# Kernel optimization log

Measured on AMD Instinct MI355X. Metric: run time of the kernel, lower is better.

## Reference

```python
import jax, jax.numpy as jnp
import numpy as np

N = 50000      # nodes
E = 800000     # edges (before self loops)
HID = 128      # hidden_dim
FEAT = 128     # feat_dim
NEG_SLOPE = 0.2
BN_EPS = 1e-5


def setup_inputs() -> dict:
    key = jax.random.key(0)
    ks = jax.random.split(key, 16)
    s = lambda d: 1.0 / np.sqrt(d).astype(np.float32)
    return {
        "x": jax.random.normal(ks[0], (N, HID), jnp.float32),
        "edge_index": jax.random.randint(ks[1], (2, E), 0, N, jnp.int32),
        # GATConv 1 (hidden -> hidden)
        "W1": jax.random.normal(ks[2], (HID, HID), jnp.float32) * s(HID),
        "att_src1": jax.random.normal(ks[3], (HID,), jnp.float32) * s(HID),
        "att_dst1": jax.random.normal(ks[4], (HID,), jnp.float32) * s(HID),
        "b1": jnp.zeros((HID,), jnp.float32),
        # BatchNorm1d(hidden) -- eval mode buffers/params
        "bn_gamma": jnp.ones((HID,), jnp.float32),
        "bn_beta": jnp.zeros((HID,), jnp.float32),
        "bn_mean": jax.random.normal(ks[5], (HID,), jnp.float32) * 0.1,
        "bn_var": jax.random.uniform(ks[6], (HID,), jnp.float32, 0.5, 1.5),
        # GATConv 2 (hidden -> feat)
        "W2": jax.random.normal(ks[7], (HID, FEAT), jnp.float32) * s(HID),
        "att_src2": jax.random.normal(ks[8], (FEAT,), jnp.float32) * s(FEAT),
        "att_dst2": jax.random.normal(ks[9], (FEAT,), jnp.float32) * s(FEAT),
        "b2": jnp.zeros((FEAT,), jnp.float32),
    }


def _gat_conv(x, W, att_src, att_dst, bias, src, dst, n_nodes):
    """PyG GATConv, heads=1: gather -> edge attn -> segment softmax -> scatter."""
    h = x @ W                                   # [N, d_out]
    a_s = h @ att_src                           # [N]
    a_d = h @ att_dst                           # [N]
    e = jax.nn.leaky_relu(a_s[src] + a_d[dst], NEG_SLOPE)  # [E']
    # numerically-stable softmax over incoming edges of each dst node
    e_max = jax.ops.segment_max(e, dst, num_segments=n_nodes)
    ex = jnp.exp(e - e_max[dst])
    denom = jax.ops.segment_sum(ex, dst, num_segments=n_nodes)
    alpha = ex / (denom[dst] + 1e-16)           # [E']
    out = jax.ops.segment_sum(alpha[:, None] * h[src], dst, num_segments=n_nodes)
    return out + bias


def reference(x, edge_index, W1, att_src1, att_dst1, b1,
              bn_gamma, bn_beta, bn_mean, bn_var,
              W2, att_src2, att_dst2, b2):
    n = x.shape[0]
    loops = jnp.arange(n, dtype=edge_index.dtype)
    src = jnp.concatenate([edge_index[0], loops])
    dst = jnp.concatenate([edge_index[1], loops])

    h = jax.nn.relu(_gat_conv(x, W1, att_src1, att_dst1, b1, src, dst, n))
    # BatchNorm1d in eval mode (running stats); dropout is identity in eval
    h = (h - bn_mean) * jax.lax.rsqrt(bn_var + BN_EPS) * bn_gamma + bn_beta
    out = jax.nn.relu(_gat_conv(h, W2, att_src2, att_dst2, b2, src, dst, n))
    return out
```

## Files before the change

### kernel.cpp

```cpp
#include <hip/hip_runtime.h>

typedef unsigned short u16;
typedef unsigned int   u32;
typedef __attribute__((ext_vector_type(8))) short bh8;
typedef __attribute__((ext_vector_type(4))) float fx4;

#define SCAN_FLAG 0x40000000

__device__ __forceinline__ float b2f(u16 h){ return __uint_as_float(((u32)h) << 16); }
__device__ __forceinline__ u16   f2b(float f){
  u32 u = __float_as_uint(f);
  u32 r = u + 0x7FFFu + ((u >> 16) & 1u);
  return (u16)(r >> 16);
}
__device__ __forceinline__ float lo16(u32 w){ return b2f((u16)(w & 0xFFFFu)); }
__device__ __forceinline__ float hi16(u32 w){ return b2f((u16)(w >> 16)); }

__global__ void r26_zero(int* __restrict__ cnt, int n1, int* __restrict__ pub){
  int g = (int)blockIdx.x*256 + threadIdx.x;
  if (g < n1) cnt[g] = 0;
  else if (g < n1 + 256) pub[g - n1] = 0;
}

__global__ void r26_hist_prep(const int* __restrict__ ei, int E, int Ep, int* cnt,
                              u16* __restrict__ rank,
                              const float* __restrict__ W1, const float* __restrict__ as1,
                              const float* __restrict__ ad1,
                              const float* __restrict__ W2, const float* __restrict__ as2,
                              const float* __restrict__ ad2,
                              u16* __restrict__ w1H, u16* __restrict__ w1L,
                              u16* __restrict__ w2H, u16* __restrict__ w2L,
                              float* __restrict__ ws1, float* __restrict__ wd1,
                              float* __restrict__ ws2, float* __restrict__ wd2){
  int b = blockIdx.x;
  int t = threadIdx.x;
  if (b < 16){
    const float* W = (b < 8) ? W1 : W2;
    u16* HT = (b < 8) ? w1H : w2H;
    u16* LT = (b < 8) ? w1L : w2L;
    int n0 = (b & 7) * 16;
    #pragma unroll
    for (int it = 0; it < 8; ++it){
      int idx = it*256 + t;
      int nn = n0 + (idx >> 7);
      int k = idx & 127;
      float w = W[(size_t)k*128 + nn];
      u16 h = f2b(w);
      HT[(size_t)nn*128 + k] = h;
      LT[(size_t)nn*128 + k] = f2b(w - b2f(h));
    }
    return;
  }
  if (b == 16){
    int which = t >> 6;
    const float* W   = (which < 2) ? W1 : W2;
    const float* att = (which == 0) ? as1 : (which == 1) ? ad1 : (which == 2) ? as2 : ad2;
    float* outv      = (which == 0) ? ws1 : (which == 1) ? wd1 : (which == 2) ? ws2 : wd2;
    int k0 = (t & 63) * 2;
    #pragma unroll
    for (int kk = 0; kk < 2; ++kk){
      int k = k0 + kk;
      float s = 0.f;
      for (int c = 0; c < 128; ++c) s = fmaf(W[(size_t)k*128 + c], att[c], s);
      outv[k] = s;
    }
    return;
  }
  int g0 = (b - 17)*2048 + t;
  #pragma unroll
  for (int i = 0; i < 8; ++i){
    int g = g0 + i*256;
    if (g < Ep){
      int dst = (g < E) ? ei[E + g] : (g - E);
      int r = atomicAdd(&cnt[dst], 1);
      rank[g] = (u16)r;
    }
  }
}

__global__ __launch_bounds__(256)
void r26_scan(const int* __restrict__ cnt, int n, int* __restrict__ offs,
              int* __restrict__ pub){
  __shared__ int tmp[256];
  __shared__ int red[256];
  int t = threadIdx.x; int b = blockIdx.x; int g = b*256 + t;
  int v = (g < n) ? cnt[g] : 0;
  tmp[t] = v; __syncthreads();
  for (int off = 1; off < 256; off <<= 1){
    int u = (t >= off) ? tmp[t - off] : 0;
    __syncthreads();
    tmp[t] += u;
    __syncthreads();
  }
  int incl = tmp[t];
  if (t == 255) atomicExch(&pub[b], tmp[255] | SCAN_FLAG);
  int val = 0;
  if (t < b){
    int p;
    do { p = atomicAdd(&pub[t], 0); } while (!(p & SCAN_FLAG));
    val = p & ~SCAN_FLAG;
  }
  red[t] = val; __syncthreads();
  for (int off = 128; off >= 1; off >>= 1){
    if (t < off) red[t] += red[t + off];
    __syncthreads();
  }
  int add = red[0];
  if (g < n) offs[g] = add + incl - v;
}

__device__ __forceinline__ void gemm16_wave(
    const float* __restrict__ X, const u16* __restrict__ wH, const u16* __restrict__ wL,
    const float* __restrict__ wsv, const float* __restrict__ wdv,
    u16* __restrict__ HB, float* __restrict__ AS, float* __restrict__ AD,
    int nrows, int w, int lane)
{
  int r0 = w * 16;
  if (r0 >= nrows) return;
  int rloc = lane & 15;
  int q    = lane >> 4;
  int myrow = r0 + rloc;
  bool act = (myrow < nrows);
  int rsafe = act ? myrow : (nrows - 1);

  fx4 acc[8] = {};
  float ds = 0.f, dd = 0.f;

  const u16* wHrow = wH + (size_t)rloc * 128;
  const u16* wLrow = wL + (size_t)rloc * 128;

  #pragma unroll
  for (int kk = 0; kk < 4; ++kk){
    int kbase = kk*32 + q*8;
    const float* xp = X + (size_t)rsafe*128 + kbase;
    float4 xa = *(const float4*)xp;
    float4 xb = *(const float4*)(xp + 4);
    float xv[8] = {xa.x, xa.y, xa.z, xa.w, xb.x, xb.y, xb.z, xb.w};
    if (!act){
      #pragma unroll
      for (int i = 0; i < 8; ++i) xv[i] = 0.f;
    }
    const float* sp = wsv + kbase;
    const float* dp = wdv + kbase;
    bh8 xh, xl;
    #pragma unroll
    for (int i = 0; i < 8; ++i){
      ds = fmaf(xv[i], sp[i], ds);
      dd = fmaf(xv[i], dp[i], dd);
      u16 h = f2b(xv[i]);
      xh[i] = (short)h;
      xl[i] = (short)f2b(xv[i] - b2f(h));
    }
    #pragma unroll
    for (int cf = 0; cf < 8; ++cf){
      bh8 wh = *(const bh8*)(wHrow + (size_t)cf*2048 + kbase);
      bh8 wl = *(const bh8*)(wLrow + (size_t)cf*2048 + kbase);
      acc[cf] = __builtin_amdgcn_mfma_f32_16x16x32_bf16(wh, xh, acc[cf], 0, 0, 0);
      acc[cf] = __builtin_amdgcn_mfma_f32_16x16x32_bf16(wl, xh, acc[cf], 0, 0, 0);
      acc[cf] = __builtin_amdgcn_mfma_f32_16x16x32_bf16(wh, xl, acc[cf], 0, 0, 0);
    }
  }
  ds += __shfl_xor(ds, 16); ds += __shfl_xor(ds, 32);
  dd += __shfl_xor(dd, 16); dd += __shfl_xor(dd, 32);
  if (act && q == 0){ AS[myrow] = ds; AD[myrow] = dd; }
  if (act){
    u16* hrow = HB + (size_t)myrow*128 + q*4;
    #pragma unroll
    for (int cf = 0; cf < 8; ++cf){
      uint2 pb;
      pb.x = (u32)f2b(acc[cf][0]) | ((u32)f2b(acc[cf][1]) << 16);
      pb.y = (u32)f2b(acc[cf][2]) | ((u32)f2b(acc[cf][3]) << 16);
      *(uint2*)(hrow + cf*16) = pb;
    }
  }
}

__global__ __launch_bounds__(256)
void r26_gemm_fill(const float* __restrict__ X,
                   const u16* __restrict__ wH, const u16* __restrict__ wL,
                   const float* __restrict__ wsv, const float* __restrict__ wdv,
                   u16* __restrict__ HB, float* __restrict__ AS, float* __restrict__ AD,
                   int nrows, int gemmBlocks,
                   const int* __restrict__ ei, int E, int Ep,
                   const int* __restrict__ offs, const u16* __restrict__ rank,
                   u16* __restrict__ csr){
  int t = threadIdx.x;
  if ((int)blockIdx.x >= gemmBlocks){
    int g0 = ((int)blockIdx.x - gemmBlocks)*1024 + t;
    #pragma unroll
    for (int i = 0; i < 4; ++i){
      int g = g0 + i*256;
      if (g < Ep){
        int src, dst;
        if (g < E){ src = ei[g]; dst = ei[E + g]; } else { src = g - E; dst = g - E; }
        csr[offs[dst] + (int)rank[g]] = (u16)src;
      }
    }
    return;
  }
  int w = (int)blockIdx.x*4 + (t >> 6);
  gemm16_wave(X, wH, wL, wsv, wdv, HB, AS, AD, nrows, w, t & 63);
}

__global__ __launch_bounds__(1024)
void r26_fused(const u16* __restrict__ HB, const float* __restrict__ AS,
               const float* __restrict__ AD,
               const int* __restrict__ offs, const u16* __restrict__ csr,
               const float* __restrict__ bias,
               const float* __restrict__ gamma_, const float* __restrict__ beta_,
               const float* __restrict__ mean_, const float* __restrict__ var_,
               const u16* __restrict__ w2H, const u16* __restrict__ w2L,
               const float* __restrict__ ws2, const float* __restrict__ wd2,
               u16* __restrict__ HB2, float* __restrict__ AS2, float* __restrict__ AD2,
               int n){
  __shared__ float xs[16*132];
  int tid  = threadIdx.x;
  int w    = tid >> 6;
  int lane = tid & 63;
  int wid  = (int)blockIdx.x*16 + w;
  bool validNode = (wid < n);
  int h  = lane >> 5;
  int c4 = (lane & 31) * 4;
  float a0 = 0.f, a1 = 0.f, a2 = 0.f, a3 = 0.f;

  if (validNode){
    int beg = offs[wid], end = offs[wid+1];
    int deg = end - beg;
    float ad = AD[wid];
    if (deg <= 64){
      int   my_s = 0;
      float my_e = -3.0e38f;
      bool act = (lane < deg);
      if (act){
        my_s = (int)csr[beg + lane];
        float e = AS[my_s] + ad;
        my_e = (e > 0.f) ? e : 0.2f*e;
      }
      float m = my_e;
      #pragma unroll
      for (int off = 32; off >= 1; off >>= 1) m = fmaxf(m, __shfl_xor(m, off));
      float pz = act ? __expf(my_e - m) : 0.f;
      float den = pz;
      #pragma unroll
      for (int off = 32; off >= 1; off >>= 1) den += __shfl_xor(den, off);
      float my_al = pz / (den + 1e-16f);

      int npair = (deg + 1) >> 1;
      int k = 0;
      for (; k + 4 <= npair; k += 4){
        int j0 = 2*k + h, j1 = j0 + 2, j2 = j0 + 4, j3 = j0 + 6;
        int   s0 = __shfl(my_s, j0),  s1 = __shfl(my_s, j1);
        int   s2 = __shfl(my_s, j2),  s3 = __shfl(my_s, j3);
        float l0 = __shfl(my_al, j0), l1 = __shfl(my_al, j1);
        float l2 = __shfl(my_al, j2), l3 = __shfl(my_al, j3);
        uint2 q0 = *(const uint2*)&HB[(size_t)s0*128 + c4];
        uint2 q1 = *(const uint2*)&HB[(size_t)s1*128 + c4];
        uint2 q2 = *(const uint2*)&HB[(size_t)s2*128 + c4];
        uint2 q3 = *(const uint2*)&HB[(size_t)s3*128 + c4];
        a0 = fmaf(l0, lo16(q0.x), a0); a1 = fmaf(l0, hi16(q0.x), a1);
        a2 = fmaf(l0, lo16(q0.y), a2); a3 = fmaf(l0, hi16(q0.y), a3);
        a0 = fmaf(l1, lo16(q1.x), a0); a1 = fmaf(l1, hi16(q1.x), a1);
        a2 = fmaf(l1, lo16(q1.y), a2); a3 = fmaf(l1, hi16(q1.y), a3);
        a0 = fmaf(l2, lo16(q2.x), a0); a1 = fmaf(l2, hi16(q2.x), a1);
        a2 = fmaf(l2, lo16(q2.y), a2); a3 = fmaf(l2, hi16(q2.y), a3);
        a0 = fmaf(l3, lo16(q3.x), a0); a1 = fmaf(l3, hi16(q3.x), a1);
        a2 = fmaf(l3, lo16(q3.y), a2); a3 = fmaf(l3, hi16(q3.y), a3);
      }
      for (; k < npair; ++k){
        int j = 2*k + h;
        int   s = __shfl(my_s, j);
        float l = __shfl(my_al, j);
        uint2 q = *(const uint2*)&HB[(size_t)s*128 + c4];
        a0 = fmaf(l, lo16(q.x), a0); a1 = fmaf(l, hi16(q.x), a1);
        a2 = fmaf(l, lo16(q.y), a2); a3 = fmaf(l, hi16(q.y), a3);
      }
    } else {
      float m = -3.0e38f;
      for (int k = beg + lane; k < end; k += 64){
        int s = (int)csr[k];
        float e = AS[s] + ad; e = (e > 0.f) ? e : 0.2f*e;
        m = fmaxf(m, e);
      }
      #pragma unroll
      for (int off = 32; off >= 1; off >>= 1) m = fmaxf(m, __shfl_xor(m, off));
      float den = 0.f;
      for (int k = beg + lane; k < end; k += 64){
        int s = (int)csr[k];
        float e = AS[s] + ad; e = (e > 0.f) ? e : 0.2f*e;
        den += __expf(e - m);
      }
      #pragma unroll
      for (int off = 32; off >= 1; off >>= 1) den += __shfl_xor(den, off);
      float inv = 1.0f / (den + 1e-16f);
      for (int j = h; j < deg; j += 2){
        int s = (int)csr[beg + j];
        float e = AS[s] + ad; e = (e > 0.f) ? e : 0.2f*e;
        float al = __expf(e - m) * inv;
        uint2 q = *(const uint2*)&HB[(size_t)s*128 + c4];
        a0 = fmaf(al, lo16(q.x), a0); a1 = fmaf(al, hi16(q.x), a1);
        a2 = fmaf(al, lo16(q.y), a2); a3 = fmaf(al, hi16(q.y), a3);
      }
    }
    a0 += __shfl_xor(a0, 32); a1 += __shfl_xor(a1, 32);
    a2 += __shfl_xor(a2, 32); a3 += __shfl_xor(a3, 32);
  }

  if (lane < 32){
    float v0 = 0.f, v1 = 0.f, v2 = 0.f, v3 = 0.f;
    if (validNode){
      float4 bv = *(const float4*)(bias + c4);
      v0 = fmaxf(a0 + bv.x, 0.f);
      v1 = fmaxf(a1 + bv.y, 0.f);
      v2 = fmaxf(a2 + bv.z, 0.f);
      v3 = fmaxf(a3 + bv.w, 0.f);
      float4 gv = *(const float4*)(gamma_ + c4);
      float4 vv = *(const float4*)(var_   + c4);
      float4 mv = *(const float4*)(mean_  + c4);
      float4 be = *(const float4*)(beta_  + c4);
      v0 = (v0 - mv.x) * (gv.x * rsqrtf(vv.x + 1e-5f)) + be.x;
      v1 = (v1 - mv.y) * (gv.y * rsqrtf(vv.y + 1e-5f)) + be.y;
      v2 = (v2 - mv.z) * (gv.z * rsqrtf(vv.z + 1e-5f)) + be.z;
      v3 = (v3 - mv.w) * (gv.w * rsqrtf(vv.w + 1e-5f)) + be.w;
    }
    float4 o = {v0, v1, v2, v3};
    *(float4*)&xs[w*132 + c4] = o;
    float4 sv = *(const float4*)(ws2 + c4);
    float4 dv = *(const float4*)(wd2 + c4);
    float ps = v0*sv.x + v1*sv.y + v2*sv.z + v3*sv.w;
    float pd = v0*dv.x + v1*dv.y + v2*dv.z + v3*dv.w;
    #pragma unroll
    for (int off = 16; off >= 1; off >>= 1){
      ps += __shfl_xor(ps, off);
      pd += __shfl_xor(pd, off);
    }
    if (lane == 0 && validNode){ AS2[wid] = ps; AD2[wid] = pd; }
  }
  __syncthreads();

  if (w >= 8) return;
  int cf   = w;
  int rloc = lane & 15;
  int q    = lane >> 4;
  int row  = (int)blockIdx.x*16 + rloc;
  fx4 acc = {0.f, 0.f, 0.f, 0.f};
  const u16* wHrow = w2H + (size_t)(cf*16 + rloc)*128;
  const u16* wLrow = w2L + (size_t)(cf*16 + rloc)*128;
  #pragma unroll
  for (int kk = 0; kk < 4; ++kk){
    int kbase = kk*32 + q*8;
    float4 xa = *(const float4*)&xs[rloc*132 + kbase];
    float4 xb = *(const float4*)&xs[rloc*132 + kbase + 4];
    float xv[8] = {xa.x, xa.y, xa.z, xa.w, xb.x, xb.y, xb.z, xb.w};
    bh8 xh, xl;
    #pragma unroll
    for (int i = 0; i < 8; ++i){
      u16 hh = f2b(xv[i]);
      xh[i] = (short)hh;
      xl[i] = (short)f2b(xv[i] - b2f(hh));
    }
    bh8 wh = *(const bh8*)(wHrow + kbase);
    bh8 wl = *(const bh8*)(wLrow + kbase);
    acc = __builtin_amdgcn_mfma_f32_16x16x32_bf16(wh, xh, acc, 0, 0, 0);
    acc = __builtin_amdgcn_mfma_f32_16x16x32_bf16(wl, xh, acc, 0, 0, 0);
    acc = __builtin_amdgcn_mfma_f32_16x16x32_bf16(wh, xl, acc, 0, 0, 0);
  }
  if (row < n){
    uint2 pb;
    pb.x = (u32)f2b(acc[0]) | ((u32)f2b(acc[1]) << 16);
    pb.y = (u32)f2b(acc[2]) | ((u32)f2b(acc[3]) << 16);
    *(uint2*)&HB2[(size_t)row*128 + q*4 + cf*16] = pb;
  }
}

__global__ __launch_bounds__(256)
void r26_aggregate(const u16* __restrict__ HB, const float* __restrict__ AS,
                   const float* __restrict__ AD,
                   const int* __restrict__ offs, const u16* __restrict__ csr,
                   const float* __restrict__ bias,
                   float* __restrict__ outp, int n){
  int wid  = (blockIdx.x*256 + threadIdx.x) >> 6;
  int lane = threadIdx.x & 63;
  if (wid >= n) return;
  int beg = offs[wid], end = offs[wid+1];
  int deg = end - beg;
  float ad = AD[wid];
  int h  = lane >> 5;
  int c4 = (lane & 31) * 4;
  float a0 = 0.f, a1 = 0.f, a2 = 0.f, a3 = 0.f;

  if (deg <= 64){
    int   my_s = 0;
    float my_e = -3.0e38f;
    bool act = (lane < deg);
    if (act){
      my_s = (int)csr[beg + lane];
      float e = AS[my_s] + ad;
      my_e = (e > 0.f) ? e : 0.2f*e;
    }
    float m = my_e;
    #pragma unroll
    for (int off = 32; off >= 1; off >>= 1) m = fmaxf(m, __shfl_xor(m, off));
    float pz = act ? __expf(my_e - m) : 0.f;
    float den = pz;
    #pragma unroll
    for (int off = 32; off >= 1; off >>= 1) den += __shfl_xor(den, off);
    float my_al = pz / (den + 1e-16f);

    int npair = (deg + 1) >> 1;
    int k = 0;
    for (; k + 4 <= npair; k += 4){
      int j0 = 2*k + h, j1 = j0 + 2, j2 = j0 + 4, j3 = j0 + 6;
      int   s0 = __shfl(my_s, j0),  s1 = __shfl(my_s, j1);
      int   s2 = __shfl(my_s, j2),  s3 = __shfl(my_s, j3);
      float l0 = __shfl(my_al, j0), l1 = __shfl(my_al, j1);
      float l2 = __shfl(my_al, j2), l3 = __shfl(my_al, j3);
      uint2 q0 = *(const uint2*)&HB[(size_t)s0*128 + c4];
      uint2 q1 = *(const uint2*)&HB[(size_t)s1*128 + c4];
      uint2 q2 = *(const uint2*)&HB[(size_t)s2*128 + c4];
      uint2 q3 = *(const uint2*)&HB[(size_t)s3*128 + c4];
      a0 = fmaf(l0, lo16(q0.x), a0); a1 = fmaf(l0, hi16(q0.x), a1);
      a2 = fmaf(l0, lo16(q0.y), a2); a3 = fmaf(l0, hi16(q0.y), a3);
      a0 = fmaf(l1, lo16(q1.x), a0); a1 = fmaf(l1, hi16(q1.x), a1);
      a2 = fmaf(l1, lo16(q1.y), a2); a3 = fmaf(l1, hi16(q1.y), a3);
      a0 = fmaf(l2, lo16(q2.x), a0); a1 = fmaf(l2, hi16(q2.x), a1);
      a2 = fmaf(l2, lo16(q2.y), a2); a3 = fmaf(l2, hi16(q2.y), a3);
      a0 = fmaf(l3, lo16(q3.x), a0); a1 = fmaf(l3, hi16(q3.x), a1);
      a2 = fmaf(l3, lo16(q3.y), a2); a3 = fmaf(l3, hi16(q3.y), a3);
    }
    for (; k < npair; ++k){
      int j = 2*k + h;
      int   s = __shfl(my_s, j);
      float l = __shfl(my_al, j);
      uint2 q = *(const uint2*)&HB[(size_t)s*128 + c4];
      a0 = fmaf(l, lo16(q.x), a0); a1 = fmaf(l, hi16(q.x), a1);
      a2 = fmaf(l, lo16(q.y), a2); a3 = fmaf(l, hi16(q.y), a3);
    }
  } else {
    float m = -3.0e38f;
    for (int k = beg + lane; k < end; k += 64){
      int s = (int)csr[k];
      float e = AS[s] + ad; e = (e > 0.f) ? e : 0.2f*e;
      m = fmaxf(m, e);
    }
    #pragma unroll
    for (int off = 32; off >= 1; off >>= 1) m = fmaxf(m, __shfl_xor(m, off));
    float den = 0.f;
    for (int k = beg + lane; k < end; k += 64){
      int s = (int)csr[k];
      float e = AS[s] + ad; e = (e > 0.f) ? e : 0.2f*e;
      den += __expf(e - m);
    }
    #pragma unroll
    for (int off = 32; off >= 1; off >>= 1) den += __shfl_xor(den, off);
    float inv = 1.0f / (den + 1e-16f);
    for (int j = h; j < deg; j += 2){
      int s = (int)csr[beg + j];
      float e = AS[s] + ad; e = (e > 0.f) ? e : 0.2f*e;
      float al = __expf(e - m) * inv;
      uint2 q = *(const uint2*)&HB[(size_t)s*128 + c4];
      a0 = fmaf(al, lo16(q.x), a0); a1 = fmaf(al, hi16(q.x), a1);
      a2 = fmaf(al, lo16(q.y), a2); a3 = fmaf(al, hi16(q.y), a3);
    }
  }

  a0 += __shfl_xor(a0, 32); a1 += __shfl_xor(a1, 32);
  a2 += __shfl_xor(a2, 32); a3 += __shfl_xor(a3, 32);
  if (lane < 32){
    float4 bv = *(const float4*)(bias + c4);
    float4 o;
    o.x = fmaxf(a0 + bv.x, 0.f);
    o.y = fmaxf(a1 + bv.y, 0.f);
    o.z = fmaxf(a2 + bv.z, 0.f);
    o.w = fmaxf(a3 + bv.w, 0.f);
    *(float4*)(outp + (size_t)wid*128 + c4) = o;
  }
}

extern "C" void kernel_launch(void* const* d_in, const int* in_sizes, int n_in,
                              void* d_out, int out_size, void* d_ws, size_t ws_size,
                              hipStream_t stream){
  const float* x   = (const float*)d_in[0];
  const int*   ei  = (const int*)  d_in[1];
  const float* W1  = (const float*)d_in[2];
  const float* as1 = (const float*)d_in[3];
  const float* ad1 = (const float*)d_in[4];
  const float* b1  = (const float*)d_in[5];
  const float* bng = (const float*)d_in[6];
  const float* bnb = (const float*)d_in[7];
  const float* bnm = (const float*)d_in[8];
  const float* bnv = (const float*)d_in[9];
  const float* W2  = (const float*)d_in[10];
  const float* as2 = (const float*)d_in[11];
  const float* ad2 = (const float*)d_in[12];
  const float* b2  = (const float*)d_in[13];
  float* out = (float*)d_out;

  int N  = in_sizes[0] / 128;
  int E  = in_sizes[1] / 2;
  int Ep = E + N;
  if (N <= 0 || E <= 0) return;

  char* base = (char*)d_ws;
  size_t off = 0;
  auto alloc = [&](size_t bytes)->char*{
    off = (off + 255) & ~(size_t)255;
    char* q = base + off; off += bytes; return q;
  };
  float* AS     = (float*)alloc((size_t)N*4);
  float* AD     = (float*)alloc((size_t)N*4);
  float* AS2    = (float*)alloc((size_t)N*4);
  float* AD2    = (float*)alloc((size_t)N*4);
  int*   cnt    = (int*)  alloc((size_t)(N+1)*4);
  int*   offs   = (int*)  alloc((size_t)(N+1)*4);
  int*   pub    = (int*)  alloc(256*4);
  u16*   rank   = (u16*)  alloc((size_t)Ep*2);
  u16*   csr    = (u16*)  alloc((size_t)Ep*2);
  u16*   hb     = (u16*)  alloc((size_t)N*128*2);
  u16*   hb2    = (u16*)  alloc((size_t)N*128*2);
  u16*   w1H    = (u16*)  alloc(128*128*2);
  u16*   w1L    = (u16*)  alloc(128*128*2);
  u16*   w2H    = (u16*)  alloc(128*128*2);
  u16*   w2L    = (u16*)  alloc(128*128*2);
  float* ws1    = (float*)alloc(128*4);
  float* wd1    = (float*)alloc(128*4);
  float* ws2    = (float*)alloc(128*4);
  float* wd2    = (float*)alloc(128*4);

  int n1  = N + 1;
  int sb  = (n1 + 255)/256;
  int zb  = (n1 + 256 + 255)/256;
  int ebH = (Ep + 2047)/2048;
  int ebF = (Ep + 1023)/1024;
  int nW  = (N + 15)/16;
  int gwb = (nW + 3)/4;
  int fb  = (N + 15)/16;
  int wb  = (N + 3)/4;

  r26_zero<<<zb, 256, 0, stream>>>(cnt, n1, pub);
  r26_hist_prep<<<17 + ebH, 256, 0, stream>>>(ei, E, Ep, cnt, rank,
                                              W1, as1, ad1, W2, as2, ad2,
                                              w1H, w1L, w2H, w2L,
                                              ws1, wd1, ws2, wd2);
  r26_scan<<<sb, 256, 0, stream>>>(cnt, n1, offs, pub);
  r26_gemm_fill<<<gwb + ebF, 256, 0, stream>>>(x, w1H, w1L, ws1, wd1,
                                               hb, AS, AD, N, gwb,
                                               ei, E, Ep, offs, rank, csr);
  r26_fused<<<fb, 1024, 0, stream>>>(hb, AS, AD, offs, csr, b1,
                                     bng, bnb, bnm, bnv,
                                     w2H, w2L, ws2, wd2,
                                     hb2, AS2, AD2, N);
  r26_aggregate<<<wb, 256, 0, stream>>>(hb2, AS2, AD2, offs, csr, b2, out, N);
}
```

Before: 289.7 us.

## Fuse scan into GEMM/fill kernel with in-kernel completion counter

```diff
diff --git a/kernel.cpp b/kernel.cpp
--- a/kernel.cpp
+++ b/kernel.cpp
@@ -16,13 +16,13 @@
 __device__ __forceinline__ float lo16(u32 w){ return b2f((u16)(w & 0xFFFFu)); }
 __device__ __forceinline__ float hi16(u32 w){ return b2f((u16)(w >> 16)); }
 
-__global__ void r26_zero(int* __restrict__ cnt, int n1, int* __restrict__ pub){
+__global__ void r27_zero(int* __restrict__ cnt, int n1, int* __restrict__ pub){
   int g = (int)blockIdx.x*256 + threadIdx.x;
   if (g < n1) cnt[g] = 0;
-  else if (g < n1 + 256) pub[g - n1] = 0;
-}
-
-__global__ void r26_hist_prep(const int* __restrict__ ei, int E, int Ep, int* cnt,
+  else if (g < n1 + 257) pub[g - n1] = 0;
+}
+
+__global__ void r27_hist_prep(const int* __restrict__ ei, int E, int Ep, int* cnt,
                               u16* __restrict__ rank,
                               const float* __restrict__ W1, const float* __restrict__ as1,
                               const float* __restrict__ ad1,
@@ -78,37 +78,6 @@
   }
 }
 
-__global__ __launch_bounds__(256)
-void r26_scan(const int* __restrict__ cnt, int n, int* __restrict__ offs,
-              int* __restrict__ pub){
-  __shared__ int tmp[256];
-  __shared__ int red[256];
-  int t = threadIdx.x; int b = blockIdx.x; int g = b*256 + t;
-  int v = (g < n) ? cnt[g] : 0;
-  tmp[t] = v; __syncthreads();
-  for (int off = 1; off < 256; off <<= 1){
-    int u = (t >= off) ? tmp[t - off] : 0;
-    __syncthreads();
-    tmp[t] += u;
-    __syncthreads();
-  }
-  int incl = tmp[t];
-  if (t == 255) atomicExch(&pub[b], tmp[255] | SCAN_FLAG);
-  int val = 0;
-  if (t < b){
-    int p;
-    do { p = atomicAdd(&pub[t], 0); } while (!(p & SCAN_FLAG));
-    val = p & ~SCAN_FLAG;
-  }
-  red[t] = val; __syncthreads();
-  for (int off = 128; off >= 1; off >>= 1){
-    if (t < off) red[t] += red[t + off];
-    __syncthreads();
-  }
-  int add = red[0];
-  if (g < n) offs[g] = add + incl - v;
-}
-
 __device__ __forceinline__ void gemm16_wave(
     const float* __restrict__ X, const u16* __restrict__ wH, const u16* __restrict__ wL,
     const float* __restrict__ wsv, const float* __restrict__ wdv,
@@ -176,34 +145,74 @@
 }
 
 __global__ __launch_bounds__(256)
-void r26_gemm_fill(const float* __restrict__ X,
-                   const u16* __restrict__ wH, const u16* __restrict__ wL,
-                   const float* __restrict__ wsv, const float* __restrict__ wdv,
-                   u16* __restrict__ HB, float* __restrict__ AS, float* __restrict__ AD,
-                   int nrows, int gemmBlocks,
-                   const int* __restrict__ ei, int E, int Ep,
-                   const int* __restrict__ offs, const u16* __restrict__ rank,
-                   u16* __restrict__ csr){
+void r27_gemm_scan_fill(const float* __restrict__ X,
+                        const u16* __restrict__ wH, const u16* __restrict__ wL,
+                        const float* __restrict__ wsv, const float* __restrict__ wdv,
+                        u16* __restrict__ HB, float* __restrict__ AS, float* __restrict__ AD,
+                        int nrows, int sb, int gemmBlocks,
+                        const int* __restrict__ ei, int E, int Ep,
+                        const int* __restrict__ cnt, int n1,
+                        int* __restrict__ offs, int* __restrict__ pub,
+                        const u16* __restrict__ rank, u16* __restrict__ csr){
+  __shared__ int tmp[256];
+  __shared__ int red[256];
   int t = threadIdx.x;
-  if ((int)blockIdx.x >= gemmBlocks){
-    int g0 = ((int)blockIdx.x - gemmBlocks)*1024 + t;
-    #pragma unroll
-    for (int i = 0; i < 4; ++i){
-      int g = g0 + i*256;
-      if (g < Ep){
-        int src, dst;
-        if (g < E){ src = ei[g]; dst = ei[E + g]; } else { src = g - E; dst = g - E; }
-        csr[offs[dst] + (int)rank[g]] = (u16)src;
-      }
-    }
+  int b = (int)blockIdx.x;
+  int* sdone = pub + 256;
+
+  if (b < sb){
+    int g = b*256 + t;
+    int v = (g < n1) ? cnt[g] : 0;
+    tmp[t] = v; __syncthreads();
+    for (int off = 1; off < 256; off <<= 1){
+      int u = (t >= off) ? tmp[t - off] : 0;
+      __syncthreads();
+      tmp[t] += u;
+      __syncthreads();
+    }
+    int incl = tmp[t];
+    if (t == 255) atomicExch(&pub[b], tmp[255] | SCAN_FLAG);
+    int val = 0;
+    if (t < b){
+      int p;
+      do { p = atomicAdd(&pub[t], 0); } while (!(p & SCAN_FLAG));
+      val = p & ~SCAN_FLAG;
+    }
+    red[t] = val; __syncthreads();
+    for (int off = 128; off >= 1; off >>= 1){
+      if (t < off) red[t] += red[t + off];
+      __syncthreads();
+    }
+    int add = red[0];
+    if (g < n1) offs[g] = add + incl - v;
+    __syncthreads();
+    if (t == 0){ __threadfence(); atomicAdd(sdone, 1); }
     return;
   }
-  int w = (int)blockIdx.x*4 + (t >> 6);
-  gemm16_wave(X, wH, wL, wsv, wdv, HB, AS, AD, nrows, w, t & 63);
+  if (b < sb + gemmBlocks){
+    int w = (b - sb)*4 + (t >> 6);
+    gemm16_wave(X, wH, wL, wsv, wdv, HB, AS, AD, nrows, w, t & 63);
+    return;
+  }
+  if (t == 0){
+    while (atomicAdd(sdone, 0) < sb) { }
+    __threadfence();
+  }
+  __syncthreads();
+  int g0 = (b - sb - gemmBlocks)*1024 + t;
+  #pragma unroll
+  for (int i = 0; i < 4; ++i){
+    int g = g0 + i*256;
+    if (g < Ep){
+      int src, dst;
+      if (g < E){ src = ei[g]; dst = ei[E + g]; } else { src = g - E; dst = g - E; }
+      csr[offs[dst] + (int)rank[g]] = (u16)src;
+    }
+  }
 }
 
 __global__ __launch_bounds__(1024)
-void r26_fused(const u16* __restrict__ HB, const float* __restrict__ AS,
+void r27_fused(const u16* __restrict__ HB, const float* __restrict__ AS,
                const float* __restrict__ AD,
                const int* __restrict__ offs, const u16* __restrict__ csr,
                const float* __restrict__ bias,
@@ -373,7 +382,7 @@
 }
 
 __global__ __launch_bounds__(256)
-void r26_aggregate(const u16* __restrict__ HB, const float* __restrict__ AS,
+void r27_aggregate(const u16* __restrict__ HB, const float* __restrict__ AS,
                    const float* __restrict__ AD,
                    const int* __restrict__ offs, const u16* __restrict__ csr,
                    const float* __restrict__ bias,
@@ -512,7 +521,7 @@
   float* AD2    = (float*)alloc((size_t)N*4);
   int*   cnt    = (int*)  alloc((size_t)(N+1)*4);
   int*   offs   = (int*)  alloc((size_t)(N+1)*4);
-  int*   pub    = (int*)  alloc(256*4);
+  int*   pub    = (int*)  alloc(257*4);
   u16*   rank   = (u16*)  alloc((size_t)Ep*2);
   u16*   csr    = (u16*)  alloc((size_t)Ep*2);
   u16*   hb     = (u16*)  alloc((size_t)N*128*2);
@@ -528,7 +537,7 @@
 
   int n1  = N + 1;
   int sb  = (n1 + 255)/256;
-  int zb  = (n1 + 256 + 255)/256;
+  int zb  = (n1 + 257 + 255)/256;
   int ebH = (Ep + 2047)/2048;
   int ebF = (Ep + 1023)/1024;
   int nW  = (N + 15)/16;
@@ -536,18 +545,18 @@
   int fb  = (N + 15)/16;
   int wb  = (N + 3)/4;
 
-  r26_zero<<<zb, 256, 0, stream>>>(cnt, n1, pub);
-  r26_hist_prep<<<17 + ebH, 256, 0, stream>>>(ei, E, Ep, cnt, rank,
+  r27_zero<<<zb, 256, 0, stream>>>(cnt, n1, pub);
+  r27_hist_prep<<<17 + ebH, 256, 0, stream>>>(ei, E, Ep, cnt, rank,
                                               W1, as1, ad1, W2, as2, ad2,
                                               w1H, w1L, w2H, w2L,
                                               ws1, wd1, ws2, wd2);
-  r26_scan<<<sb, 256, 0, stream>>>(cnt, n1, offs, pub);
-  r26_gemm_fill<<<gwb + ebF, 256, 0, stream>>>(x, w1H, w1L, ws1, wd1,
-                                               hb, AS, AD, N, gwb,
-                                               ei, E, Ep, offs, rank, csr);
-  r26_fused<<<fb, 1024, 0, stream>>>(hb, AS, AD, offs, csr, b1,
+  r27_gemm_scan_fill<<<sb + gwb + ebF, 256, 0, stream>>>(x, w1H, w1L, ws1, wd1,
+                                                         hb, AS, AD, N, sb, gwb,
+                                                         ei, E, Ep, cnt, n1,
+                                                         offs, pub, rank, csr);
+  r27_fused<<<fb, 1024, 0, stream>>>(hb, AS, AD, offs, csr, b1,
                                      bng, bnb, bnm, bnv,
                                      w2H, w2L, ws2, wd2,
                                      hb2, AS2, AD2, N);
-  r26_aggregate<<<wb, 256, 0, stream>>>(hb2, AS2, AD2, offs, csr, b2, out, N);
-}
+  r27_aggregate<<<wb, 256, 0, stream>>>(hb2, AS2, AD2, offs, csr, b2, out, N);
+}
```

Measured after the change: 320.7 us. +10.7%, slower.
